# Kernel optimization log

Measured on AMD Instinct MI355X. Metric: run time of the kernel, lower is better.

Reference implementation:

```python
import jax, jax.numpy as jnp
import numpy as np

N = 10000      # nodes
E = 640000     # edges
P = 500000     # OD training pairs
IN, HID, EMB = 128, 256, 64


def _graph_conv(x, W, b, src, dst, norm_out, norm_in):
    # DGL GraphConv, norm='both': y = D_in^{-1/2} A (D_out^{-1/2} x) W + b
    h = x * norm_out[:, None]
    agg = jax.ops.segment_sum(h[src], dst, num_segments=N)  # [N, d]
    return agg * norm_in[:, None] @ W + b


def setup_inputs() -> dict:
    key = jax.random.key(0)
    ks = jax.random.split(key, 13)
    x = jax.random.normal(ks[0], (N, IN), jnp.float32)
    dis = jax.random.uniform(ks[1], (N, N), jnp.float32)
    src = jax.random.randint(ks[2], (E,), 0, N, dtype=jnp.int64)
    dst = jax.random.randint(ks[3], (E,), 0, N, dtype=jnp.int64)
    train_idx = jax.random.randint(ks[4], (2, P), 0, N, dtype=jnp.int64)

    def w(k, i, o):
        return (jax.random.normal(k, (i, o), jnp.float32) / np.sqrt(i)).astype(jnp.float32)

    return {
        'x': x, 'dis': dis,
        'W1': w(ks[5], IN, HID),  'b1': jnp.zeros((HID,), jnp.float32),
        'W2': w(ks[6], HID, HID), 'b2': jnp.zeros((HID,), jnp.float32),
        'W3': w(ks[7], HID, EMB), 'b3': jnp.zeros((EMB,), jnp.float32),
        'Wout': w(ks[8], 2 * EMB + 1, 1), 'bout': jnp.zeros((1,), jnp.float32),
        'src': src, 'dst': dst, 'train_idx': train_idx,
    }


def reference(x, dis, W1, b1, W2, b2, W3, b3, Wout, bout, src, dst, train_idx):
    ones = jnp.ones((E,), x.dtype)
    deg_out = jax.ops.segment_sum(ones, src, num_segments=N)
    deg_in = jax.ops.segment_sum(ones, dst, num_segments=N)
    norm_out = jnp.where(deg_out > 0, jax.lax.rsqrt(jnp.maximum(deg_out, 1.0)), 0.0)
    norm_in = jnp.where(deg_in > 0, jax.lax.rsqrt(jnp.maximum(deg_in, 1.0)), 0.0)

    h = jax.nn.relu(_graph_conv(x, W1, b1, src, dst, norm_out, norm_in))
    h = jax.nn.relu(_graph_conv(h, W2, b2, src, dst, norm_out, norm_in))
    g_emb = jax.nn.sigmoid(_graph_conv(h, W3, b3, src, dst, norm_out, norm_in))  # [N, EMB]

    o_emb = g_emb[train_idx[0]]                      # [P, EMB]
    d_emb = g_emb[train_idx[1]]                      # [P, EMB]
    dis_emb = dis[train_idx[0], train_idx[1]][:, None]  # [P, 1]
    emb = jnp.concatenate((o_emb, d_emb, dis_emb), axis=1)  # [P, 2*EMB+1]
    return jnp.tanh(emb @ Wout + bout)               # [P, 1]
```

## Files before the change

kernel.cpp:

```cpp
#include <hip/hip_runtime.h>
#include <math.h>

typedef __attribute__((ext_vector_type(8))) short short8;
typedef __attribute__((ext_vector_type(8))) unsigned short ushort8;
typedef __attribute__((ext_vector_type(4))) float f32x4;

#define NTHR 256
#define CAP 192

__device__ __forceinline__ ushort f2bf(float f) {
    uint u = __float_as_uint(f);
    return (ushort)((u + 0x7FFFu + ((u >> 16) & 1u)) >> 16);
}
__device__ __forceinline__ uint pk2bf(float a, float b) {
    return (uint)f2bf(a) | ((uint)f2bf(b) << 16);
}
__device__ __forceinline__ float bfl(uint r) { return __uint_as_float(r << 16); }
__device__ __forceinline__ float bfh(uint r) { return __uint_as_float(r & 0xFFFF0000u); }

struct Params {
    const float* x; const float* dis;
    const float* W1; const float* b1;
    const float* W2; const float* b2;
    const float* W3; const float* b3;
    const float* Wout; const float* bout;
    const int* src; const int* dst; const int* ti;
    float* out;
    uint* degOut; uint* fill;
    float* normOut; float* normIn;
    ushort* ebkt;
    ushort* xbf; ushort* w1bf; ushort* w2bf; ushort* w3bf;
    ushort* bufA; ushort* bufB; ushort* bufC;
    float* av; float* bv;
    int N, E, P;
};

__global__ __launch_bounds__(NTHR) void k_pre(Params p) {
    int gtid = blockIdx.x * NTHR + threadIdx.x;
    int GSZ = gridDim.x * NTHR;
    for (int i = gtid; i < p.N; i += GSZ) {
        p.degOut[i] = 0u;
        p.fill[i] = 0u;
    }
    if (gtid < 64) ((uint*)&p.xbf[(size_t)p.N * 128])[gtid] = 0u;
    else if (gtid < 192) ((uint*)&p.bufB[(size_t)p.N * 256])[gtid - 64] = 0u;
    else if (gtid < 224) ((uint*)&p.bufC[(size_t)p.N * 64])[gtid - 192] = 0u;
    const int n1 = 128 * 256, n2 = 256 * 256, n3 = 256 * 64;
    int nw4 = (n1 + n2 + n3) >> 2;
    for (int i4 = gtid; i4 < nw4; i4 += GSZ) {
        int i = i4 * 4;
        const float* s;
        ushort* d;
        int off;
        if (i < n1) { s = p.W1; d = p.w1bf; off = i; }
        else if (i < n1 + n2) { s = p.W2; d = p.w2bf; off = i - n1; }
        else { s = p.W3; d = p.w3bf; off = i - n1 - n2; }
        float4 v = *(const float4*)&s[off];
        uint2 pkv;
        pkv.x = pk2bf(v.x, v.y);
        pkv.y = pk2bf(v.z, v.w);
        *(uint2*)&d[off] = pkv;
    }
}

__global__ __launch_bounds__(NTHR) void k_deg_scatter(Params p) {
    int e = (blockIdx.x * NTHR + threadIdx.x) * 2;
    if (e + 1 < p.E) {
        int2 s2 = *(const int2*)&p.src[e];
        int2 d2 = *(const int2*)&p.dst[e];
        atomicAdd(&p.degOut[s2.x], 1u);
        atomicAdd(&p.degOut[s2.y], 1u);
        uint p0 = atomicAdd(&p.fill[d2.x], 1u);
        p.ebkt[(size_t)d2.x * CAP + p0] = (ushort)s2.x;
        uint p1 = atomicAdd(&p.fill[d2.y], 1u);
        p.ebkt[(size_t)d2.y * CAP + p1] = (ushort)s2.y;
    } else if (e < p.E) {
        int s = p.src[e];
        int v = p.dst[e];
        atomicAdd(&p.degOut[s], 1u);
        uint pos = atomicAdd(&p.fill[v], 1u);
        p.ebkt[(size_t)v * CAP + pos] = (ushort)s;
    }
}

__global__ __launch_bounds__(NTHR) void k_norm_cvt(Params p) {
    int gtid = blockIdx.x * NTHR + threadIdx.x;
    int GSZ = gridDim.x * NTHR;
    for (int v = gtid; v < p.N; v += GSZ) {
        uint d0 = p.degOut[v];
        uint d1 = p.fill[v];
        p.normOut[v] = d0 ? rsqrtf((float)d0) : 0.f;
        p.normIn[v] = d1 ? rsqrtf((float)d1) : 0.f;
        uint c8 = (d1 + 7) & ~7u;
        ushort* eb = p.ebkt + (size_t)v * CAP;
        for (uint j = d1; j < c8; ++j) eb[j] = (ushort)p.N;
    }
    int nx4 = p.N * 32;
    for (int i4 = gtid; i4 < nx4; i4 += GSZ) {
        int i = i4 * 4;
        int row = i >> 7;
        uint d0 = p.degOut[row];
        float no = d0 ? rsqrtf((float)d0) : 0.f;
        float4 v = *(const float4*)&p.x[i];
        uint2 pkv;
        pkv.x = pk2bf(v.x * no, v.y * no);
        pkv.y = pk2bf(v.z * no, v.w * no);
        *(uint2*)&p.xbf[i] = pkv;
    }
}

template <int V> struct GT;
template <> struct GT<1> { using T = ushort; };
template <> struct GT<2> { using T = uint; };

template <int V>
__device__ __forceinline__ void accum(float* acc, typename GT<V>::T g) {
    if constexpr (V == 1) {
        acc[0] += bfl((uint)g);
    } else {
        acc[0] += bfl(g);
        acc[1] += bfh(g);
    }
}

template <int D, int SPLIT, int ACT>
__global__ __launch_bounds__(NTHR) void k_agg(Params p, const ushort* __restrict__ h,
                                              ushort* __restrict__ outb) {
    constexpr int V = D / (64 * SPLIT);
    using T = typename GT<V>::T;
    int wib = threadIdx.x >> 6;
    int b = blockIdx.x;
    int v, half;
    if constexpr (SPLIT == 2) {
        half = b & 1;
        v = (b >> 1) * 4 + wib;
    } else {
        half = 0;
        v = b * 4 + wib;
    }
    if (v >= p.N) return;
    int l = threadIdx.x & 63;
    const ushort* hb = h + half * (64 * V) + l * V;
    const ushort* eb = p.ebkt + (size_t)v * CAP;

    int cnt = (int)p.fill[v];
    float nin = p.normIn[v];
    float acc[V] = {};

    if (cnt > 0) {
        int ngrp = (cnt + 7) >> 3;
        ushort8 w = *(const ushort8*)eb;
        T gp[8];
#pragma unroll
        for (int j = 0; j < 8; ++j) gp[j] = *(const T*)&hb[(int)w[j] * D];
        for (int g = 1; g < ngrp; ++g) {
            ushort8 wn = *(const ushort8*)(eb + g * 8);
            T gn[8];
#pragma unroll
            for (int j = 0; j < 8; ++j) gn[j] = *(const T*)&hb[(int)wn[j] * D];
#pragma unroll
            for (int j = 0; j < 8; ++j) accum<V>(acc, gp[j]);
#pragma unroll
            for (int j = 0; j < 8; ++j) gp[j] = gn[j];
        }
#pragma unroll
        for (int j = 0; j < 8; ++j) accum<V>(acc, gp[j]);
    }

    if constexpr (ACT == 0) {
        static_assert(V == 2, "ACT0 expects V==2");
        *(uint*)&outb[(size_t)v * D + half * (64 * V) + l * V] =
            pk2bf(acc[0] * nin, acc[1] * nin);
    } else {
        float g = acc[0] * nin + p.b3[l];
        g = 1.f / (1.f + __expf(-g));
        float pa = g * p.Wout[l];
        float pb = g * p.Wout[64 + l];
#pragma unroll
        for (int off = 32; off > 0; off >>= 1) {
            pa += __shfl_down(pa, off);
            pb += __shfl_down(pb, off);
        }
        if (l == 0) {
            p.av[v] = pa;
            p.bv[v] = pb;
        }
    }
}

template <int BM, int K, bool RELU, bool BIAS, bool SCALE>
__global__ __launch_bounds__(256) void gemm_nf(const ushort* __restrict__ A,
                                               const ushort* __restrict__ B,
                                               const float* __restrict__ bias,
                                               const float* __restrict__ rowScale,
                                               ushort* __restrict__ C,
                                               int M, int Nn) {
    constexpr int WR = BM / 64;
    constexpr int LB = K + 8;
    __shared__ ushort Bs[64 * LB];

    int tid = threadIdx.x;
    int wave = tid >> 6;
    int lane = tid & 63;
    int l15 = lane & 15;
    int l4 = lane >> 4;
    int m0 = blockIdx.x * BM;
    int n0 = blockIdx.y * 64;

    {
        int j8 = (tid & 7) * 8;
#pragma unroll
        for (int kk = tid >> 3; kk < K; kk += 32) {
            short8 v = *(const short8*)&B[(size_t)kk * Nn + n0 + j8];
#pragma unroll
            for (int j = 0; j < 8; ++j) Bs[(j8 + j) * LB + kk] = (ushort)v[j];
        }
    }
    __syncthreads();

    f32x4 acc[WR][4] = {};
    int rowl[WR];
    const ushort* Ab[WR];
#pragma unroll
    for (int r = 0; r < WR; ++r) {
        rowl[r] = m0 + wave * (16 * WR) + r * 16 + l15;
        Ab[r] = A + (size_t)rowl[r] * K + l4 * 8;
    }

#pragma unroll
    for (int k0 = 0; k0 < K; k0 += 32) {
        short8 bf[4];
#pragma unroll
        for (int n = 0; n < 4; ++n)
            bf[n] = *(const short8*)&Bs[(n * 16 + l15) * LB + k0 + l4 * 8];
#pragma unroll
        for (int r = 0; r < WR; ++r) {
            short8 af = {};
            if (rowl[r] < M) af = *(const short8*)&Ab[r][k0];
#pragma unroll
            for (int n = 0; n < 4; ++n)
                acc[r][n] = __builtin_amdgcn_mfma_f32_16x16x32_bf16(af, bf[n], acc[r][n], 0, 0, 0);
        }
    }

#pragma unroll
    for (int r = 0; r < WR; ++r) {
        int rowb = m0 + wave * (16 * WR) + r * 16 + l4 * 4;
#pragma unroll
        for (int q = 0; q < 4; ++q) {
            int row = rowb + q;
            if (row >= M) continue;
            float sc = SCALE ? rowScale[row] : 1.f;
#pragma unroll
            for (int n = 0; n < 4; ++n) {
                int col = n0 + n * 16 + l15;
                float vv = acc[r][n][q];
                if (BIAS) vv += bias[col];
                if (RELU) vv = fmaxf(vv, 0.f);
                vv *= sc;
                C[(size_t)row * Nn + col] = f2bf(vv);
            }
        }
    }
}

__global__ __launch_bounds__(NTHR) void k_final(Params p) {
    int i = (blockIdx.x * NTHR + threadIdx.x) * 2;
    float w128 = p.Wout[128];
    float b0 = p.bout[0];
    if (i + 1 < p.P) {
        int2 o2 = *(const int2*)&p.ti[i];
        int2 d2 = *(const int2*)&p.ti[p.P + i];
        float dis0 = p.dis[(size_t)o2.x * p.N + d2.x];
        float dis1 = p.dis[(size_t)o2.y * p.N + d2.y];
        float s0 = p.av[o2.x] + p.bv[d2.x] + dis0 * w128 + b0;
        float s1 = p.av[o2.y] + p.bv[d2.y] + dis1 * w128 + b0;
        float2 r = make_float2(tanhf(s0), tanhf(s1));
        *(float2*)&p.out[i] = r;
    } else if (i < p.P) {
        int o = p.ti[i];
        int d = p.ti[p.P + i];
        float s = p.av[o] + p.bv[d] + p.dis[(size_t)o * p.N + d] * w128 + b0;
        p.out[i] = tanhf(s);
    }
}

extern "C" void kernel_launch(void* const* d_in, const int* in_sizes, int n_in,
                              void* d_out, int out_size, void* d_ws, size_t ws_size,
                              hipStream_t stream) {
    Params prm;
    prm.x    = (const float*)d_in[0];
    prm.dis  = (const float*)d_in[1];
    prm.W1   = (const float*)d_in[2];
    prm.b1   = (const float*)d_in[3];
    prm.W2   = (const float*)d_in[4];
    prm.b2   = (const float*)d_in[5];
    prm.W3   = (const float*)d_in[6];
    prm.b3   = (const float*)d_in[7];
    prm.Wout = (const float*)d_in[8];
    prm.bout = (const float*)d_in[9];
    prm.src  = (const int*)d_in[10];
    prm.dst  = (const int*)d_in[11];
    prm.ti   = (const int*)d_in[12];
    prm.out  = (float*)d_out;

    const int IN = 128, HID = 256, EMB = 64;
    prm.N = in_sizes[0] / IN;
    prm.E = in_sizes[10];
    prm.P = in_sizes[12] / 2;
    const int N = prm.N, E = prm.E, P = prm.P;

    char* ws = (char*)d_ws;
    size_t off = 0;
    auto alloc = [&](size_t bytes) {
        size_t o = off;
        off = (off + bytes + 255) & ~(size_t)255;
        return o;
    };
    size_t o_degO = alloc((size_t)N * 4);
    size_t o_fill = alloc((size_t)N * 4);
    size_t o_nrmO = alloc((size_t)N * 4);
    size_t o_nrmI = alloc((size_t)N * 4);
    size_t o_ebkt = alloc((size_t)N * CAP * 2);
    size_t o_xbf  = alloc((size_t)(N + 1) * IN * 2);
    size_t o_w1   = alloc((size_t)IN * HID * 2);
    size_t o_w2   = alloc((size_t)HID * HID * 2);
    size_t o_w3   = alloc((size_t)HID * EMB * 2);
    size_t o_bufA = alloc((size_t)N * HID * 2);
    size_t o_bufB = alloc((size_t)(N + 1) * HID * 2);
    size_t o_bufC = alloc((size_t)(N + 1) * EMB * 2);
    size_t o_av   = alloc((size_t)N * 4);
    size_t o_bv   = alloc((size_t)N * 4);
    (void)ws_size;

    prm.degOut  = (uint*)(ws + o_degO);
    prm.fill    = (uint*)(ws + o_fill);
    prm.normOut = (float*)(ws + o_nrmO);
    prm.normIn  = (float*)(ws + o_nrmI);
    prm.ebkt    = (ushort*)(ws + o_ebkt);
    prm.xbf     = (ushort*)(ws + o_xbf);
    prm.w1bf    = (ushort*)(ws + o_w1);
    prm.w2bf    = (ushort*)(ws + o_w2);
    prm.w3bf    = (ushort*)(ws + o_w3);
    prm.bufA    = (ushort*)(ws + o_bufA);
    prm.bufB    = (ushort*)(ws + o_bufB);
    prm.bufC    = (ushort*)(ws + o_bufC);
    prm.av      = (float*)(ws + o_av);
    prm.bv      = (float*)(ws + o_bv);

    k_pre<<<256, NTHR, 0, stream>>>(prm);
    k_deg_scatter<<<(E / 2 + NTHR - 1) / NTHR, NTHR, 0, stream>>>(prm);
    k_norm_cvt<<<1024, NTHR, 0, stream>>>(prm);

    int nb4 = (N + 3) / 4;

    k_agg<128, 1, 0><<<nb4, NTHR, 0, stream>>>(prm, prm.xbf, prm.bufA);
    {
        dim3 grid((N + 127) / 128, HID / 64);
        gemm_nf<128, 128, true, true, true><<<grid, 256, 0, stream>>>(
            prm.bufA, prm.w1bf, prm.b1, prm.normOut, prm.bufB, N, HID);
    }
    k_agg<256, 2, 0><<<nb4 * 2, NTHR, 0, stream>>>(prm, prm.bufB, prm.bufA);
    {
        dim3 grid((N + 127) / 128, HID / 64);
        gemm_nf<128, 256, true, true, true><<<grid, 256, 0, stream>>>(
            prm.bufA, prm.w2bf, prm.b2, prm.normOut, prm.bufB, N, HID);
    }
    {
        dim3 grid((N + 63) / 64, EMB / 64);
        gemm_nf<64, 256, false, false, false><<<grid, 256, 0, stream>>>(
            prm.bufB, prm.w3bf, nullptr, nullptr, prm.bufC, N, EMB);
    }
    k_agg<64, 1, 2><<<nb4, NTHR, 0, stream>>>(prm, prm.bufC, nullptr);
    k_final<<<(P / 2 + NTHR - 1) / NTHR, NTHR, 0, stream>>>(prm);
}
```

Before: 170.0 us.

## Fuse layer-2 and layer-3 GEMMs into one kernel keeping intermediate in LDS

Replaces the two separate GEMM launches (W2 with bias/relu/norm scaling, then W3) with a single kernel that computes a 64-row tile of the 256-wide hidden activation into shared memory and immediately multiplies it by W3. This removes the global write and re-read of the N x 256 intermediate and one kernel launch. In exchange, each block reloads and transposes all of W2 and W3 into LDS, uses about 66KB of shared memory which limits occupancy, and runs only about 157 blocks. It also makes minor cleanups (merged count buffers, a generalized agg store path).

```diff
diff --git a/kernel.cpp b/kernel.cpp
--- a/kernel.cpp
+++ b/kernel.cpp
@@ -29,8 +29,11 @@
     uint* degOut; uint* fill;
     float* normOut; float* normIn;
     ushort* ebkt;
-    ushort* xbf; ushort* w1bf; ushort* w2bf; ushort* w3bf;
-    ushort* bufA; ushort* bufB; ushort* bufC;
+    ushort* xbf;
+    ushort* w1bf; ushort* w2bf; ushort* w3bf;
+    ushort* bufA;
+    ushort* bufB;
+    ushort* bufC;
     float* av; float* bv;
     int N, E, P;
 };
@@ -168,9 +171,12 @@
     }
 
     if constexpr (ACT == 0) {
-        static_assert(V == 2, "ACT0 expects V==2");
-        *(uint*)&outb[(size_t)v * D + half * (64 * V) + l * V] =
-            pk2bf(acc[0] * nin, acc[1] * nin);
+        if constexpr (V == 2) {
+            *(uint*)&outb[(size_t)v * D + half * (64 * V) + l * V] =
+                pk2bf(acc[0] * nin, acc[1] * nin);
+        } else {
+            outb[(size_t)v * D + half * 64 + l] = f2bf(acc[0] * nin);
+        }
     } else {
         float g = acc[0] * nin + p.b3[l];
         g = 1.f / (1.f + __expf(-g));
@@ -259,6 +265,94 @@
                 if (RELU) vv = fmaxf(vv, 0.f);
                 vv *= sc;
                 C[(size_t)row * Nn + col] = f2bf(vv);
+            }
+        }
+    }
+}
+
+__global__ __launch_bounds__(256) void k_gemm23(Params p) {
+    constexpr int LB = 264;
+    __shared__ ushort Bs[64 * LB];
+    __shared__ ushort Cs[64 * LB];
+
+    int tid = threadIdx.x;
+    int wave = tid >> 6;
+    int lane = tid & 63;
+    int l15 = lane & 15, l4 = lane >> 4;
+    int m0 = blockIdx.x * 64;
+
+    int rowA = m0 + wave * 16 + l15;
+    bool rok = rowA < p.N;
+    const ushort* Ab = p.bufA + (size_t)rowA * 256 + l4 * 8;
+
+    for (int c = 0; c < 4; ++c) {
+        {
+            int j8 = (tid & 7) * 8;
+#pragma unroll
+            for (int kk = tid >> 3; kk < 256; kk += 32) {
+                short8 v = *(const short8*)&p.w2bf[(size_t)kk * 256 + c * 64 + j8];
+#pragma unroll
+                for (int j = 0; j < 8; ++j) Bs[(j8 + j) * LB + kk] = (ushort)v[j];
+            }
+        }
+        __syncthreads();
+
+        f32x4 acc[4] = {};
+#pragma unroll
+        for (int k0 = 0; k0 < 256; k0 += 32) {
+            short8 af = {};
+            if (rok) af = *(const short8*)&Ab[k0];
+#pragma unroll
+            for (int n = 0; n < 4; ++n) {
+                short8 bf = *(const short8*)&Bs[(n * 16 + l15) * LB + k0 + l4 * 8];
+                acc[n] = __builtin_amdgcn_mfma_f32_16x16x32_bf16(af, bf, acc[n], 0, 0, 0);
+            }
+        }
+#pragma unroll
+        for (int n = 0; n < 4; ++n) {
+            int col = c * 64 + n * 16 + l15;
+            float bs = p.b2[col];
+#pragma unroll
+            for (int q = 0; q < 4; ++q) {
+                int rl = wave * 16 + l4 * 4 + q;
+                int grow = m0 + rl;
+                float no = (grow < p.N) ? p.normOut[grow] : 0.f;
+                Cs[rl * LB + col] = f2bf(fmaxf(acc[n][q] + bs, 0.f) * no);
+            }
+        }
+        __syncthreads();
+    }
+
+    {
+        int j8 = (tid & 7) * 8;
+#pragma unroll
+        for (int kk = tid >> 3; kk < 256; kk += 32) {
+            short8 v = *(const short8*)&p.w3bf[(size_t)kk * 64 + j8];
+#pragma unroll
+            for (int j = 0; j < 8; ++j) Bs[(j8 + j) * LB + kk] = (ushort)v[j];
+        }
+    }
+    __syncthreads();
+
+    {
+        f32x4 acc[4] = {};
+        const ushort* arow = &Cs[(wave * 16 + l15) * LB + l4 * 8];
+#pragma unroll
+        for (int k0 = 0; k0 < 256; k0 += 32) {
+            short8 af = *(const short8*)&arow[k0];
+#pragma unroll
+            for (int n = 0; n < 4; ++n) {
+                short8 bf = *(const short8*)&Bs[(n * 16 + l15) * LB + k0 + l4 * 8];
+                acc[n] = __builtin_amdgcn_mfma_f32_16x16x32_bf16(af, bf, acc[n], 0, 0, 0);
+            }
+        }
+#pragma unroll
+        for (int n = 0; n < 4; ++n) {
+            int col = n * 16 + l15;
+#pragma unroll
+            for (int q = 0; q < 4; ++q) {
+                int grow = m0 + wave * 16 + l4 * 4 + q;
+                if (grow < p.N) p.bufC[(size_t)grow * 64 + col] = f2bf(acc[n][q]);
             }
         }
     }
@@ -317,8 +411,7 @@
         off = (off + bytes + 255) & ~(size_t)255;
         return o;
     };
-    size_t o_degO = alloc((size_t)N * 4);
-    size_t o_fill = alloc((size_t)N * 4);
+    size_t o_cnts = alloc((size_t)2 * N * 4);
     size_t o_nrmO = alloc((size_t)N * 4);
     size_t o_nrmI = alloc((size_t)N * 4);
     size_t o_ebkt = alloc((size_t)N * CAP * 2);
@@ -333,8 +426,8 @@
     size_t o_bv   = alloc((size_t)N * 4);
     (void)ws_size;
 
-    prm.degOut  = (uint*)(ws + o_degO);
-    prm.fill    = (uint*)(ws + o_fill);
+    prm.degOut  = (uint*)(ws + o_cnts);
+    prm.fill    = prm.degOut + N;
     prm.normOut = (float*)(ws + o_nrmO);
     prm.normIn  = (float*)(ws + o_nrmI);
     prm.ebkt    = (ushort*)(ws + o_ebkt);
@@ -361,16 +454,7 @@
             prm.bufA, prm.w1bf, prm.b1, prm.normOut, prm.bufB, N, HID);
     }
     k_agg<256, 2, 0><<<nb4 * 2, NTHR, 0, stream>>>(prm, prm.bufB, prm.bufA);
-    {
-        dim3 grid((N + 127) / 128, HID / 64);
-        gemm_nf<128, 256, true, true, true><<<grid, 256, 0, stream>>>(
-            prm.bufA, prm.w2bf, prm.b2, prm.normOut, prm.bufB, N, HID);
-    }
-    {
-        dim3 grid((N + 63) / 64, EMB / 64);
-        gemm_nf<64, 256, false, false, false><<<grid, 256, 0, stream>>>(
-            prm.bufB, prm.w3bf, nullptr, nullptr, prm.bufC, N, EMB);
-    }
+    k_gemm23<<<(N + 63) / 64, 256, 0, stream>>>(prm);
     k_agg<64, 1, 2><<<nb4, NTHR, 0, stream>>>(prm, prm.bufC, nullptr);
     k_final<<<(P / 2 + NTHR - 1) / NTHR, NTHR, 0, stream>>>(prm);
 }
```

New measurement: 174.1 us. 2.4% more time.
